# Optimization experiments

Hardware: AMD Instinct MI355X
Metric: run time of the kernel (lower is better)

## Reference

```python
import jax, jax.numpy as jnp
import numpy as np

R = 5  # box filter radius (self.r)
EPS = 0.01


def box_filter(x, r):
    # depthwise (groups=C) box filter, kernel (2r+1)x(2r+1), zero padding r
    c = x.shape[1]
    k = 2 * r + 1
    w = jnp.full((c, 1, k, k), 1.0 / (k * k), dtype=x.dtype)
    return jax.lax.conv_general_dilated(
        x, w, window_strides=(1, 1), padding=[(r, r), (r, r)],
        dimension_numbers=("NCHW", "OIHW", "NCHW"), feature_group_count=c)


def setup_inputs() -> dict:
    key = jax.random.key(0)
    x = jax.random.normal(key, (4, 64, 256, 256), dtype=jnp.float32)
    return {"x": x}


def reference(x):
    _, _, H, W = x.shape
    # normalization map accounting for zero-padded borders
    N = box_filter(jnp.ones((1, 1, H, W), dtype=x.dtype), R)  # [1,1,H,W]
    mean_x = box_filter(x, R) / N
    var_x = box_filter(x * x, R) / N - mean_x * mean_x
    A = var_x / (var_x + EPS)
    b = (1.0 - A) * mean_x
    m = A * x + b
    return x * m
```

## Files before the change

kernel.cpp:

```cpp
#include <hip/hip_runtime.h>
#include <hip/hip_bf16.h>


#define RAD    5
#define KW     11
#define IMG_H  256
#define IMG_W  256
#define TILE_H 8
#define IN_H   (TILE_H + 2 * RAD)
#define STRIPS (IMG_H / TILE_H)
#define EPS_F  0.01f

__global__ __launch_bounds__(256)
void AdaGuidedFilter_17686675325295_kernel(const float* __restrict__ x,
                                           float* __restrict__ out) {
    __shared__ float2 vsum[TILE_H * IMG_W];

    const int d     = blockIdx.x;
    const int L     = (d & 7) * ((256 * STRIPS) / 8) + (d >> 3);
    const int img   = L >> 5;
    const int strip = L & (STRIPS - 1);
    const int tid   = threadIdx.x;

    const float* __restrict__ xim = x   + (size_t)img * (IMG_H * IMG_W);
    float* __restrict__       oim = out + (size_t)img * (IMG_H * IMG_W);

    const int row0 = strip * TILE_H - RAD;

    {
        float xr[IN_H];
        if (strip != 0 && strip != STRIPS - 1) {
            #pragma unroll
            for (int li = 0; li < IN_H; ++li)
                xr[li] = xim[(size_t)(row0 + li) * IMG_W + tid];
        } else {
            #pragma unroll
            for (int li = 0; li < IN_H; ++li) {
                const int g = row0 + li;
                xr[li] = (g >= 0 && g < IMG_H) ? xim[(size_t)g * IMG_W + tid] : 0.0f;
            }
        }

        float s = 0.0f, s2 = 0.0f;
        #pragma unroll
        for (int li = 0; li < KW; ++li) { s += xr[li]; s2 = fmaf(xr[li], xr[li], s2); }

        #pragma unroll
        for (int r = 0; r < TILE_H; ++r) {
            vsum[(r << 8) | (tid ^ r)] = make_float2(s, s2);
            if (r < TILE_H - 1) {
                const float a = xr[r + KW], b0 = xr[r];
                s  += a - b0;
                s2 += a * a - b0 * b0;
            }
        }
    }
    __syncthreads();

    const int lr  = tid & 7;
    const int seg = tid >> 3;
    const int c0  = seg * 8;
    const int gr  = strip * TILE_H + lr;

    float xv[8];
    {
        const float4* p = reinterpret_cast<const float4*>(xim + (size_t)gr * IMG_W + c0);
        const float4 q0 = p[0], q1 = p[1];
        xv[0]=q0.x; xv[1]=q0.y; xv[2]=q0.z; xv[3]=q0.w;
        xv[4]=q1.x; xv[5]=q1.y; xv[6]=q1.z; xv[7]=q1.w;
    }

    const int rlo = (gr - RAD < 0) ? 0 : gr - RAD;
    const int rhi = (gr + RAD > IMG_H - 1) ? IMG_H - 1 : gr + RAD;
    const float rcnt = (float)(rhi - rlo + 1);

    float o[8];
    if (seg >= 1 && seg <= 30) {
        float s = 0.0f, s2 = 0.0f;
        #pragma unroll
        for (int dd = -RAD; dd <= RAD; ++dd) {
            const float2 v = vsum[(lr << 8) | ((c0 + dd) ^ lr)];
            s += v.x; s2 += v.y;
        }
        const float inv = __builtin_amdgcn_rcpf(rcnt * 11.0f);
        #pragma unroll
        for (int i = 0; i < 8; ++i) {
            const float mean = s * inv;
            const float m2   = s2 * inv;
            const float var  = fmaf(-mean, mean, m2);
            const float A    = var * __builtin_amdgcn_rcpf(var + EPS_F);
            const float xq   = xv[i];
            o[i] = xq * fmaf(A, xq - mean, mean);
            if (i < 7) {
                const float2 va = vsum[(lr << 8) | ((c0 + i + RAD + 1) ^ lr)];
                const float2 vb = vsum[(lr << 8) | ((c0 + i - RAD) ^ lr)];
                s  += va.x - vb.x;
                s2 += va.y - vb.y;
            }
        }
    } else {
        float s = 0.0f, s2 = 0.0f;
        #pragma unroll
        for (int dd = -RAD; dd <= RAD; ++dd) {
            const int cc = c0 + dd;
            if (cc >= 0 && cc < IMG_W) {
                const float2 v = vsum[(lr << 8) | (cc ^ lr)];
                s += v.x; s2 += v.y;
            }
        }
        #pragma unroll
        for (int i = 0; i < 8; ++i) {
            const int c   = c0 + i;
            const int wlo = (c - RAD < 0) ? 0 : c - RAD;
            const int whi = (c + RAD > IMG_W - 1) ? IMG_W - 1 : c + RAD;
            const float inv  = __builtin_amdgcn_rcpf(rcnt * (float)(whi - wlo + 1));
            const float mean = s * inv;
            const float m2   = s2 * inv;
            const float var  = fmaf(-mean, mean, m2);
            const float A    = var * __builtin_amdgcn_rcpf(var + EPS_F);
            const float xq   = xv[i];
            o[i] = xq * fmaf(A, xq - mean, mean);
            if (i < 7) {
                const int ca = c + RAD + 1;
                const int cs = c - RAD;
                if (ca < IMG_W) { const float2 v = vsum[(lr << 8) | (ca ^ lr)]; s += v.x; s2 += v.y; }
                if (cs >= 0)    { const float2 v = vsum[(lr << 8) | (cs ^ lr)]; s -= v.x; s2 -= v.y; }
            }
        }
    }

    float4* orow = reinterpret_cast<float4*>(oim + (size_t)gr * IMG_W + c0);
    orow[0] = make_float4(o[0], o[1], o[2], o[3]);
    orow[1] = make_float4(o[4], o[5], o[6], o[7]);
}

extern "C" void kernel_launch(void* const* d_in, const int* in_sizes, int n_in,
                              void* d_out, int out_size, void* d_ws, size_t ws_size,
                              hipStream_t stream) {
    (void)in_sizes; (void)n_in; (void)d_ws; (void)ws_size; (void)out_size;
    const float* x = (const float*)d_in[0];
    float* out = (float*)d_out;
    dim3 grid(256 * STRIPS);
    dim3 block(256);
    AdaGuidedFilter_17686675325295_kernel<<<grid, block, 0, stream>>>(x, out);
}
```

Measured before the change: 29.13 us.

## Halve strip height to 4 rows and template the border row check

Reduces the rows per block from 8 to 4, doubling the grid to 16384 blocks. Each thread now computes 4 output columns instead of 8, and the strip body is templated so only edge strips carry row-bounds checks. The global load of x for the output rows is also moved ahead of the barrier. The aim is more parallelism and overlap, but it raises halo re-reading of input from 18/8 to 14/4 rows per output row, adding global/L2 traffic on a memory-bound kernel.

```diff
diff --git a/kernel.cpp b/kernel.cpp
--- a/kernel.cpp
+++ b/kernel.cpp
@@ -6,76 +6,60 @@
 #define KW     11
 #define IMG_H  256
 #define IMG_W  256
-#define TILE_H 8
+#define TILE_H 4
 #define IN_H   (TILE_H + 2 * RAD)
 #define STRIPS (IMG_H / TILE_H)
+#define NBLK   (256 * STRIPS)
 #define EPS_F  0.01f
 
-__global__ __launch_bounds__(256)
-void AdaGuidedFilter_17686675325295_kernel(const float* __restrict__ x,
-                                           float* __restrict__ out) {
-    __shared__ float2 vsum[TILE_H * IMG_W];
-
-    const int d     = blockIdx.x;
-    const int L     = (d & 7) * ((256 * STRIPS) / 8) + (d >> 3);
-    const int img   = L >> 5;
-    const int strip = L & (STRIPS - 1);
-    const int tid   = threadIdx.x;
-
-    const float* __restrict__ xim = x   + (size_t)img * (IMG_H * IMG_W);
-    float* __restrict__       oim = out + (size_t)img * (IMG_H * IMG_W);
-
+template<bool ROWCHECK>
+__device__ __forceinline__ void run_strip(const float* __restrict__ xim,
+                                          float* __restrict__ oim,
+                                          float2* __restrict__ vsum,
+                                          int strip, int t) {
     const int row0 = strip * TILE_H - RAD;
 
     {
         float xr[IN_H];
-        if (strip != 0 && strip != STRIPS - 1) {
-            #pragma unroll
-            for (int li = 0; li < IN_H; ++li)
-                xr[li] = xim[(size_t)(row0 + li) * IMG_W + tid];
-        } else {
-            #pragma unroll
-            for (int li = 0; li < IN_H; ++li) {
-                const int g = row0 + li;
-                xr[li] = (g >= 0 && g < IMG_H) ? xim[(size_t)g * IMG_W + tid] : 0.0f;
-            }
+        #pragma unroll
+        for (int li = 0; li < IN_H; ++li) {
+            const int g = row0 + li;
+            xr[li] = (!ROWCHECK || ((unsigned)g < (unsigned)IMG_H))
+                       ? xim[(size_t)g * IMG_W + t] : 0.0f;
         }
-
         float s = 0.0f, s2 = 0.0f;
         #pragma unroll
         for (int li = 0; li < KW; ++li) { s += xr[li]; s2 = fmaf(xr[li], xr[li], s2); }
-
         #pragma unroll
         for (int r = 0; r < TILE_H; ++r) {
-            vsum[(r << 8) | (tid ^ r)] = make_float2(s, s2);
+            vsum[(r << 8) | (t ^ r)] = make_float2(s, s2);
             if (r < TILE_H - 1) {
-                const float a = xr[r + KW], b0 = xr[r];
-                s  += a - b0;
-                s2 += a * a - b0 * b0;
+                const float a = xr[r + KW], b = xr[r];
+                s  += a - b;
+                s2  = fmaf(a, a, fmaf(-b, b, s2));
             }
         }
     }
-    __syncthreads();
 
-    const int lr  = tid & 7;
-    const int seg = tid >> 3;
-    const int c0  = seg * 8;
+    const int lr  = t & 3;
+    const int seg = t >> 2;
+    const int c0  = seg << 2;
     const int gr  = strip * TILE_H + lr;
 
-    float xv[8];
+    float xv[4];
     {
-        const float4* p = reinterpret_cast<const float4*>(xim + (size_t)gr * IMG_W + c0);
-        const float4 q0 = p[0], q1 = p[1];
-        xv[0]=q0.x; xv[1]=q0.y; xv[2]=q0.z; xv[3]=q0.w;
-        xv[4]=q1.x; xv[5]=q1.y; xv[6]=q1.z; xv[7]=q1.w;
+        const float4 q = *reinterpret_cast<const float4*>(xim + (size_t)gr * IMG_W + c0);
+        xv[0] = q.x; xv[1] = q.y; xv[2] = q.z; xv[3] = q.w;
     }
+
+    __syncthreads();
 
     const int rlo = (gr - RAD < 0) ? 0 : gr - RAD;
     const int rhi = (gr + RAD > IMG_H - 1) ? IMG_H - 1 : gr + RAD;
     const float rcnt = (float)(rhi - rlo + 1);
 
-    float o[8];
-    if (seg >= 1 && seg <= 30) {
+    float o[4];
+    if (seg >= 2 && seg <= 61) {
         float s = 0.0f, s2 = 0.0f;
         #pragma unroll
         for (int dd = -RAD; dd <= RAD; ++dd) {
@@ -84,14 +68,14 @@
         }
         const float inv = __builtin_amdgcn_rcpf(rcnt * 11.0f);
         #pragma unroll
-        for (int i = 0; i < 8; ++i) {
+        for (int i = 0; i < 4; ++i) {
             const float mean = s * inv;
             const float m2   = s2 * inv;
             const float var  = fmaf(-mean, mean, m2);
             const float A    = var * __builtin_amdgcn_rcpf(var + EPS_F);
             const float xq   = xv[i];
             o[i] = xq * fmaf(A, xq - mean, mean);
-            if (i < 7) {
+            if (i < 3) {
                 const float2 va = vsum[(lr << 8) | ((c0 + i + RAD + 1) ^ lr)];
                 const float2 vb = vsum[(lr << 8) | ((c0 + i - RAD) ^ lr)];
                 s  += va.x - vb.x;
@@ -109,7 +93,7 @@
             }
         }
         #pragma unroll
-        for (int i = 0; i < 8; ++i) {
+        for (int i = 0; i < 4; ++i) {
             const int c   = c0 + i;
             const int wlo = (c - RAD < 0) ? 0 : c - RAD;
             const int whi = (c + RAD > IMG_W - 1) ? IMG_W - 1 : c + RAD;
@@ -120,7 +104,7 @@
             const float A    = var * __builtin_amdgcn_rcpf(var + EPS_F);
             const float xq   = xv[i];
             o[i] = xq * fmaf(A, xq - mean, mean);
-            if (i < 7) {
+            if (i < 3) {
                 const int ca = c + RAD + 1;
                 const int cs = c - RAD;
                 if (ca < IMG_W) { const float2 v = vsum[(lr << 8) | (ca ^ lr)]; s += v.x; s2 += v.y; }
@@ -129,9 +113,28 @@
         }
     }
 
-    float4* orow = reinterpret_cast<float4*>(oim + (size_t)gr * IMG_W + c0);
-    orow[0] = make_float4(o[0], o[1], o[2], o[3]);
-    orow[1] = make_float4(o[4], o[5], o[6], o[7]);
+    *reinterpret_cast<float4*>(oim + (size_t)gr * IMG_W + c0) =
+        make_float4(o[0], o[1], o[2], o[3]);
+}
+
+__global__ __launch_bounds__(256)
+void AdaGuidedFilter_17686675325295_kernel(const float* __restrict__ x,
+                                           float* __restrict__ out) {
+    __shared__ float2 vsum[TILE_H * IMG_W];
+
+    const int d     = blockIdx.x;
+    const int L     = (d & 7) * (NBLK / 8) + (d >> 3);
+    const int img   = L >> 6;
+    const int strip = L & (STRIPS - 1);
+    const int t     = threadIdx.x;
+
+    const float* __restrict__ xim = x   + (size_t)img * (IMG_H * IMG_W);
+    float* __restrict__       oim = out + (size_t)img * (IMG_H * IMG_W);
+
+    if (strip >= 2 && strip <= STRIPS - 3)
+        run_strip<false>(xim, oim, vsum, strip, t);
+    else
+        run_strip<true>(xim, oim, vsum, strip, t);
 }
 
 extern "C" void kernel_launch(void* const* d_in, const int* in_sizes, int n_in,
@@ -140,7 +143,7 @@
     (void)in_sizes; (void)n_in; (void)d_ws; (void)ws_size; (void)out_size;
     const float* x = (const float*)d_in[0];
     float* out = (float*)d_out;
-    dim3 grid(256 * STRIPS);
+    dim3 grid(NBLK);
     dim3 block(256);
     AdaGuidedFilter_17686675325295_kernel<<<grid, block, 0, stream>>>(x, out);
 }
```

New measurement: 30.84 us. 1.06x slower.
